# Optimization experiments

Hardware: AMD Instinct MI355X
Metric: run time of the kernel (lower is better)

The kernel has to match this reference:

```python
import jax, jax.numpy as jnp
import numpy as np

B, S, DM = 4, 2048, 512
H, D = 8, 64          # att_head, head_dim = att_dim // att_head
LEFT, RIGHT = 128, 128  # band_part(left_mask, right_mask)
LARGE = 1e30          # masked_softmax large number for fp32


def setup_inputs() -> dict:
    key = jax.random.key(0)
    ks = jax.random.split(key, 11)
    scale = 1.0 / np.sqrt(DM)
    x = jax.random.normal(ks[0], (B, S, DM), jnp.float32)
    Wq = jax.random.normal(ks[1], (DM, DM), jnp.float32) * scale
    bq = jnp.zeros((DM,), jnp.float32)
    Wk = jax.random.normal(ks[2], (DM, DM), jnp.float32) * scale
    bk = jnp.zeros((DM,), jnp.float32)
    Wv = jax.random.normal(ks[3], (DM, DM), jnp.float32) * scale
    bv = jnp.zeros((DM,), jnp.float32)
    Wo = jax.random.normal(ks[4], (DM, DM), jnp.float32) * scale
    bo = jnp.zeros((DM,), jnp.float32)
    x_len = jax.random.randint(ks[5], (B,), 0, 2048)
    return {"x": x, "Wq": Wq, "bq": bq, "Wk": Wk, "bk": bk,
            "Wv": Wv, "bv": bv, "Wo": Wo, "bo": bo, "x_len": x_len}


def reference(x, Wq, bq, Wk, bk, Wv, bv, Wo, bo, x_len):
    b, s, _ = x.shape
    # QKV projections, split into heads: [B,S,H,D]
    q = (x @ Wq + bq).reshape(b, s, H, D)
    k = (x @ Wk + bk).reshape(b, s, H, D)
    v = (x @ Wv + bv).reshape(b, s, H, D)
    # content energy: [B,H,Q,K], scaled by sqrt(head_dim)
    energy = jnp.einsum('bind,bjnd->bnij', q, k) / jnp.sqrt(jnp.float32(D))
    # banded mask (tf.linalg.band_part semantics): keep -LEFT <= j-i <= RIGHT
    i = jnp.arange(s)[:, None]
    j = jnp.arange(s)[None, :]
    band = ((j - i) <= RIGHT) & ((i - j) <= LEFT)            # [S,S]
    # key-length mask (tf.sequence_mask, expanded to [B,1,1,S])
    seq = jnp.arange(s)[None, :] < x_len[:, None]            # [B,S]
    mask = (band[None, None, :, :] & seq[:, None, None, :]).astype(energy.dtype)
    # masked softmax: energy - (1 - mask) * LARGE, softmax over keys
    att = jax.nn.softmax(energy - (1.0 - mask) * LARGE, axis=-1)
    # context: [B,Q,H,D] -> [B,S,H*D]
    ctx = jnp.einsum('bnij,bjnd->bind', att, v).reshape(b, s, H * D)
    # output projection (use_proj=True)
    return ctx @ Wo + bo
```

## Files before the change

kernel.cpp:

```cpp
#include <hip/hip_runtime.h>

#define S_LEN 2048
#define BATCH 4
#define DMODEL 512
#define NHEAD 8
#define HDIM 64
#define ROWS (BATCH * S_LEN)

using short8 = __attribute__((ext_vector_type(8))) short;
using f32x4  = __attribute__((ext_vector_type(4))) float;

__device__ __forceinline__ unsigned short f2bf(float f) {
  unsigned int u = __builtin_bit_cast(unsigned int, f);
  u += 0x7fffu + ((u >> 16) & 1u);
  return (unsigned short)(u >> 16);
}
__device__ __forceinline__ float bf2f(unsigned short h) {
  unsigned int u = ((unsigned int)h) << 16;
  return __builtin_bit_cast(float, u);
}
__device__ __forceinline__ void glds16(const void* g, void* l) {
  __builtin_amdgcn_global_load_lds((const __attribute__((address_space(1))) unsigned*)g,
                                   (__attribute__((address_space(3))) unsigned*)l, 16, 0, 0);
}

__global__ __launch_bounds__(256) void prep_kernel(const float* __restrict__ x,
                                                   const float* __restrict__ Wq,
                                                   const float* __restrict__ Wk,
                                                   const float* __restrict__ Wv,
                                                   const float* __restrict__ Wo,
                                                   unsigned short* __restrict__ xb,
                                                   unsigned short* __restrict__ WqkT,
                                                   unsigned short* __restrict__ WvT,
                                                   unsigned short* __restrict__ WoT) {
  __shared__ float t[32][33];
  const int blk = blockIdx.x, tid = threadIdx.x;
  if (blk < 2048) {
    const int base = (blk * 256 + tid) * 8;
    float4 f0 = *(const float4*)(x + base);
    float4 f1 = *(const float4*)(x + base + 4);
    uint4 o;
    o.x = (unsigned)f2bf(f0.x) | ((unsigned)f2bf(f0.y) << 16);
    o.y = (unsigned)f2bf(f0.z) | ((unsigned)f2bf(f0.w) << 16);
    o.z = (unsigned)f2bf(f1.x) | ((unsigned)f2bf(f1.y) << 16);
    o.w = (unsigned)f2bf(f1.z) | ((unsigned)f2bf(f1.w) << 16);
    *(uint4*)(xb + base) = o;
    return;
  }
  const int tb = blk - 2048;
  const int which = tb >> 8;
  const int tile = tb & 255;
  const float* W = which == 0 ? Wq : which == 1 ? Wk : which == 2 ? Wv : Wo;
  unsigned short* WT = which == 0 ? WqkT : which == 1 ? (WqkT + 512 * 512)
                      : which == 2 ? WvT : WoT;
  const int tx = tid & 31, ty = tid >> 5;
  const int x0 = (tile & 15) * 32, y0 = (tile >> 4) * 32;
#pragma unroll
  for (int r = 0; r < 4; r++)
    t[ty + 8 * r][tx] = W[(size_t)(y0 + ty + 8 * r) * DMODEL + x0 + tx];
  __syncthreads();
#pragma unroll
  for (int r = 0; r < 4; r++)
    WT[(size_t)(x0 + ty + 8 * r) * DMODEL + y0 + tx] = f2bf(t[tx][ty + 8 * r]);
}

__global__ __launch_bounds__(256, 2) void gemm_qkv_kernel(const unsigned short* __restrict__ xb,
                                                          const unsigned short* __restrict__ WqkT,
                                                          const unsigned short* __restrict__ WvT,
                                                          const float* __restrict__ bq,
                                                          const float* __restrict__ bk,
                                                          const float* __restrict__ bv,
                                                          const int* __restrict__ x_len,
                                                          unsigned short* __restrict__ Qb,
                                                          unsigned short* __restrict__ Kb,
                                                          unsigned short* __restrict__ Vt) {
  constexpr int K = DMODEL;
  __shared__ __align__(16) char smem[16384];
  char* As = smem;
  char* Bs = smem + 8192;
  const int bid = blockIdx.x;
  const bool vmode = bid < 256;
  const unsigned short *A, *Bt;
  int m0, n0;
  if (vmode) {
    m0 = (bid & 3) * 128;
    n0 = (bid >> 2) * 128;
    A = WvT; Bt = xb;
  } else {
    const int q = bid - 256;
    m0 = (q >> 3) * 128;
    n0 = (q & 7) * 128;
    A = xb; Bt = WqkT;
    const int xl = x_len[m0 >> 11];
    const int s0 = m0 & 2047;
    if (n0 >= DMODEL) { if (s0 >= xl) return; }
    else if (s0 >= xl + 128) return;
  }
  const int tid = threadIdx.x;
  const int wave = tid >> 6, lane = tid & 63;
  const int wr = wave >> 1, wc = wave & 1;
  const int lm = lane & 15, lq = lane >> 4;
  const int lr = lane >> 2;
  const int lc = (lane & 3) ^ ((lane >> 3) & 3);
  const unsigned short* gA0 = A + (size_t)(m0 + wave * 16 + lr) * K + lc * 8;
  const unsigned short* gA1 = A + (size_t)(m0 + (wave + 4) * 16 + lr) * K + lc * 8;
  const unsigned short* gB0 = Bt + (size_t)(n0 + wave * 16 + lr) * K + lc * 8;
  const unsigned short* gB1 = Bt + (size_t)(n0 + (wave + 4) * 16 + lr) * K + lc * 8;
  char* lA0 = As + wave * 1024 + lane * 16;
  char* lA1 = As + (wave + 4) * 1024 + lane * 16;
  char* lB0 = Bs + wave * 1024 + lane * 16;
  char* lB1 = Bs + (wave + 4) * 1024 + lane * 16;
  const int sw = (lm >> 1) & 3;
  int aoff[4], boff[4];
#pragma unroll
  for (int mi = 0; mi < 4; mi++)
    aoff[mi] = (wr * 64 + mi * 16 + lm) * 64 + (lq ^ sw) * 16;
#pragma unroll
  for (int ni = 0; ni < 4; ni++)
    boff[ni] = (wc * 64 + ni * 16 + lm) * 64 + (lq ^ sw) * 16;

  f32x4 acc[4][4] = {};
  for (int k0 = 0; k0 < K; k0 += 32) {
    __syncthreads();
    glds16(gA0 + k0, lA0);
    glds16(gA1 + k0, lA1);
    glds16(gB0 + k0, lB0);
    glds16(gB1 + k0, lB1);
    __syncthreads();
    short8 af[4], bfr[4];
#pragma unroll
    for (int mi = 0; mi < 4; mi++) af[mi] = *(const short8*)(As + aoff[mi]);
#pragma unroll
    for (int ni = 0; ni < 4; ni++) bfr[ni] = *(const short8*)(Bs + boff[ni]);
#pragma unroll
    for (int mi = 0; mi < 4; mi++)
#pragma unroll
      for (int ni = 0; ni < 4; ni++)
        acc[mi][ni] = __builtin_amdgcn_mfma_f32_16x16x32_bf16(af[mi], bfr[ni], acc[mi][ni], 0, 0, 0);
  }
#pragma unroll
  for (int mi = 0; mi < 4; mi++) {
    const int row0 = m0 + wr * 64 + mi * 16 + lq * 4;
#pragma unroll
    for (int ni = 0; ni < 4; ni++) {
      const int col = n0 + wc * 64 + ni * 16 + lm;
#pragma unroll
      for (int r = 0; r < 4; r++) {
        const int row = row0 + r;
        const float v = acc[mi][ni][r];
        if (vmode) {
          Vt[(size_t)row * ROWS + col] = f2bf(v + bv[row]);
        } else if (col < DMODEL) {
          Qb[(size_t)row * DMODEL + col] = f2bf(v + bq[col]);
        } else {
          Kb[(size_t)row * DMODEL + (col - DMODEL)] = f2bf(v + bk[col - DMODEL]);
        }
      }
    }
  }
}

__global__ __launch_bounds__(256, 2) void gemm_out_kernel(const unsigned short* __restrict__ A,
                                                          const unsigned short* __restrict__ Bt,
                                                          const float* __restrict__ bias,
                                                          float* __restrict__ out) {
  constexpr int K = DMODEL;
  __shared__ __align__(16) char smem[16384];
  char* As = smem;
  char* Bs = smem + 8192;
  const int tid = threadIdx.x;
  const int wave = tid >> 6, lane = tid & 63;
  const int wr = wave >> 1, wc = wave & 1;
  const int lm = lane & 15, lq = lane >> 4;
  const int m0 = blockIdx.y * 128, n0 = blockIdx.x * 128;
  const int lr = lane >> 2;
  const int lc = (lane & 3) ^ ((lane >> 3) & 3);
  const unsigned short* gA0 = A + (size_t)(m0 + wave * 16 + lr) * K + lc * 8;
  const unsigned short* gA1 = A + (size_t)(m0 + (wave + 4) * 16 + lr) * K + lc * 8;
  const unsigned short* gB0 = Bt + (size_t)(n0 + wave * 16 + lr) * K + lc * 8;
  const unsigned short* gB1 = Bt + (size_t)(n0 + (wave + 4) * 16 + lr) * K + lc * 8;
  char* lA0 = As + wave * 1024 + lane * 16;
  char* lA1 = As + (wave + 4) * 1024 + lane * 16;
  char* lB0 = Bs + wave * 1024 + lane * 16;
  char* lB1 = Bs + (wave + 4) * 1024 + lane * 16;
  const int sw = (lm >> 1) & 3;
  int aoff[4], boff[4];
#pragma unroll
  for (int mi = 0; mi < 4; mi++)
    aoff[mi] = (wr * 64 + mi * 16 + lm) * 64 + (lq ^ sw) * 16;
#pragma unroll
  for (int ni = 0; ni < 4; ni++)
    boff[ni] = (wc * 64 + ni * 16 + lm) * 64 + (lq ^ sw) * 16;

  f32x4 acc[4][4] = {};
  for (int k0 = 0; k0 < K; k0 += 32) {
    __syncthreads();
    glds16(gA0 + k0, lA0);
    glds16(gA1 + k0, lA1);
    glds16(gB0 + k0, lB0);
    glds16(gB1 + k0, lB1);
    __syncthreads();
    short8 af[4], bfr[4];
#pragma unroll
    for (int mi = 0; mi < 4; mi++) af[mi] = *(const short8*)(As + aoff[mi]);
#pragma unroll
    for (int ni = 0; ni < 4; ni++) bfr[ni] = *(const short8*)(Bs + boff[ni]);
#pragma unroll
    for (int mi = 0; mi < 4; mi++)
#pragma unroll
      for (int ni = 0; ni < 4; ni++)
        acc[mi][ni] = __builtin_amdgcn_mfma_f32_16x16x32_bf16(af[mi], bfr[ni], acc[mi][ni], 0, 0, 0);
  }
#pragma unroll
  for (int mi = 0; mi < 4; mi++) {
    const int row0 = m0 + wr * 64 + mi * 16 + lq * 4;
#pragma unroll
    for (int ni = 0; ni < 4; ni++) {
      const int col = n0 + wc * 64 + ni * 16 + lm;
#pragma unroll
      for (int r = 0; r < 4; r++)
        out[(size_t)(row0 + r) * DMODEL + col] = acc[mi][ni][r] + bias[col];
    }
  }
}

__global__ __launch_bounds__(256) void vsum_kernel(const unsigned short* __restrict__ Vt,
                                                   float* __restrict__ vs) {
  const int wid = blockIdx.x * 4 + (threadIdx.x >> 6);
  const int lane = threadIdx.x & 63;
  const int b = wid >> 9, n = wid & 511;
  const unsigned short* row = Vt + (size_t)n * ROWS + b * S_LEN;
  float s = 0.f;
#pragma unroll
  for (int it = 0; it < 4; it++) {
    uint4 v = *(const uint4*)(row + it * 512 + lane * 8);
    unsigned int w[4] = {v.x, v.y, v.z, v.w};
#pragma unroll
    for (int e = 0; e < 4; e++) {
      s += bf2f((unsigned short)(w[e] & 0xffffu));
      s += bf2f((unsigned short)(w[e] >> 16));
    }
  }
#pragma unroll
  for (int off = 1; off < 64; off <<= 1) s += __shfl_xor(s, off, 64);
  if (lane == 0) vs[(size_t)b * DMODEL + n] = s;
}

__global__ __launch_bounds__(256) void attn_kernel(const unsigned short* __restrict__ Q,
                                                   const unsigned short* __restrict__ K,
                                                   const unsigned short* __restrict__ Vt,
                                                   const int* __restrict__ x_len,
                                                   const float* __restrict__ vsum,
                                                   unsigned short* __restrict__ ctx) {
  __shared__ unsigned short Ks[32][72];
  __shared__ unsigned short Vs[64][40];
  __shared__ unsigned short Ps[4][2][16][40];
  const int tid = threadIdx.x;
  const int wave = tid >> 6, lane = tid & 63;
  const int lm = lane & 15, lq = lane >> 4;
  const int b = blockIdx.z, h = blockIdx.y;
  const int i0 = blockIdx.x * 128;
  const int qbase = i0 + wave * 32;
  const int xlen = x_len[b];

  short8 aq[2][2];
#pragma unroll
  for (int g = 0; g < 2; g++) {
    const size_t qoff = (size_t)(b * S_LEN + qbase + g * 16 + lm) * DMODEL + h * HDIM + lq * 8;
    aq[g][0] = *(const short8*)(Q + qoff);
    aq[g][1] = *(const short8*)(Q + qoff + 32);
  }

  const int krow = tid >> 3, kchk = (tid & 7) * 8;
  const int vdim = tid >> 2, vchk = (tid & 3) * 8;

  f32x4 oacc[2][4] = {};
  float mrow[2][4], lrow[2][4];
#pragma unroll
  for (int g = 0; g < 2; g++)
#pragma unroll
    for (int r = 0; r < 4; r++) { mrow[g][r] = -1e30f; lrow[g][r] = 0.f; }

  for (int kt = 0; kt < 12; kt++) {
    const int jt0 = i0 - 128 + kt * 32;
    if (jt0 + 31 < 0 || jt0 >= xlen) continue;
    __syncthreads();
    {
      const int jr = jt0 + krow;
      const int jrc = min(max(jr, 0), S_LEN - 1);
      *(uint4*)&Ks[krow][kchk] =
          *(const uint4*)(K + (size_t)(b * S_LEN + jrc) * DMODEL + h * HDIM + kchk);
      const int jv = jt0 + vchk;
      const int jvc = min(max(jv, 0), S_LEN - 8);
      *(uint4*)&Vs[vdim][vchk] =
          *(const uint4*)(Vt + (size_t)(h * HDIM + vdim) * ROWS + b * S_LEN + jvc);
    }
    __syncthreads();
    if (jt0 + 159 < qbase || jt0 > qbase + 159) continue;

#pragma unroll
    for (int g = 0; g < 2; g++) {
      const int qg = qbase + g * 16;
      if (jt0 + 31 < qg - 128 || jt0 > qg + 143) continue;
      f32x4 sv[2];
#pragma unroll
      for (int sub = 0; sub < 2; sub++) {
        const short8 bk0 = *(const short8*)&Ks[sub * 16 + lm][lq * 8];
        const short8 bk1 = *(const short8*)&Ks[sub * 16 + lm][32 + lq * 8];
        f32x4 s = {};
        s = __builtin_amdgcn_mfma_f32_16x16x32_bf16(aq[g][0], bk0, s, 0, 0, 0);
        s = __builtin_amdgcn_mfma_f32_16x16x32_bf16(aq[g][1], bk1, s, 0, 0, 0);
        sv[sub] = s;
      }
#pragma unroll
      for (int sub = 0; sub < 2; sub++) {
        const int j = jt0 + sub * 16 + lm;
        const bool jv = (j >= 0) && (j < xlen);
#pragma unroll
        for (int r = 0; r < 4; r++) {
          const int i = qg + lq * 4 + r;
          const bool ok = jv && (j - i <= 128) && (i - j <= 128);
          sv[sub][r] = ok ? sv[sub][r] * 0.125f : -1e30f;
        }
      }
      float alpha[4], p0[4], p1[4];
#pragma unroll
      for (int r = 0; r < 4; r++) {
        float mx = fmaxf(sv[0][r], sv[1][r]);
#pragma unroll
        for (int off = 1; off < 16; off <<= 1) mx = fmaxf(mx, __shfl_xor(mx, off, 64));
        const float mn = fmaxf(mrow[g][r], mx);
        alpha[r] = __expf(mrow[g][r] - mn);
        mrow[g][r] = mn;
        p0[r] = (sv[0][r] > -1e29f) ? __expf(sv[0][r] - mn) : 0.f;
        p1[r] = (sv[1][r] > -1e29f) ? __expf(sv[1][r] - mn) : 0.f;
        float rs = p0[r] + p1[r];
#pragma unroll
        for (int off = 1; off < 16; off <<= 1) rs += __shfl_xor(rs, off, 64);
        lrow[g][r] = lrow[g][r] * alpha[r] + rs;
      }
#pragma unroll
      for (int r = 0; r < 4; r++) {
        Ps[wave][g][lq * 4 + r][lm] = f2bf(p0[r]);
        Ps[wave][g][lq * 4 + r][16 + lm] = f2bf(p1[r]);
      }
      const short8 pf = *(const short8*)&Ps[wave][g][lm][lq * 8];
#pragma unroll
      for (int dt = 0; dt < 4; dt++) {
#pragma unroll
        for (int r = 0; r < 4; r++) oacc[g][dt][r] *= alpha[r];
        const short8 bv = *(const short8*)&Vs[dt * 16 + lm][lq * 8];
        oacc[g][dt] = __builtin_amdgcn_mfma_f32_16x16x32_bf16(pf, bv, oacc[g][dt], 0, 0, 0);
      }
    }
  }
#pragma unroll
  for (int g = 0; g < 2; g++)
#pragma unroll
    for (int r = 0; r < 4; r++) {
      const int i = qbase + g * 16 + lq * 4 + r;
      const size_t obase = (size_t)(b * S_LEN + i) * DMODEL + h * HDIM;
      if (lrow[g][r] > 0.f) {
        const float inv = 1.f / lrow[g][r];
#pragma unroll
        for (int dt = 0; dt < 4; dt++)
          ctx[obase + dt * 16 + lm] = f2bf(oacc[g][dt][r] * inv);
      } else {
#pragma unroll
        for (int dt = 0; dt < 4; dt++)
          ctx[obase + dt * 16 + lm] =
              f2bf(vsum[(size_t)b * DMODEL + h * HDIM + dt * 16 + lm] * (1.f / 2048.f));
      }
    }
}

extern "C" void kernel_launch(void* const* d_in, const int* in_sizes, int n_in,
                              void* d_out, int out_size, void* d_ws, size_t ws_size,
                              hipStream_t stream) {
  (void)in_sizes; (void)n_in; (void)out_size; (void)ws_size;
  const float* x  = (const float*)d_in[0];
  const float* Wq = (const float*)d_in[1];
  const float* bq = (const float*)d_in[2];
  const float* Wk = (const float*)d_in[3];
  const float* bk = (const float*)d_in[4];
  const float* Wv = (const float*)d_in[5];
  const float* bv = (const float*)d_in[6];
  const float* Wo = (const float*)d_in[7];
  const float* bo = (const float*)d_in[8];
  const int* x_len = (const int*)d_in[9];

  char* ws = (char*)d_ws;
  const size_t MB = 1024 * 1024;
  unsigned short* xb   = (unsigned short*)(ws + 0 * MB);
  unsigned short* Qb   = (unsigned short*)(ws + 8 * MB);
  unsigned short* Kb   = (unsigned short*)(ws + 16 * MB);
  unsigned short* Vt   = (unsigned short*)(ws + 24 * MB);
  unsigned short* Cx   = (unsigned short*)(ws + 32 * MB);
  unsigned short* WqkT = (unsigned short*)(ws + 40 * MB);
  unsigned short* WvT  = (unsigned short*)(ws + 41 * MB);
  unsigned short* WoT  = (unsigned short*)(ws + 41 * MB + 512 * 1024);
  float* vsum          = (float*)(ws + 42 * MB);

  prep_kernel<<<3072, 256, 0, stream>>>(x, Wq, Wk, Wv, Wo, xb, WqkT, WvT, WoT);
  gemm_qkv_kernel<<<768, 256, 0, stream>>>(xb, WqkT, WvT, bq, bk, bv, x_len, Qb, Kb, Vt);
  vsum_kernel<<<512, 256, 0, stream>>>(Vt, vsum);
  attn_kernel<<<dim3(16, 8, 4), 256, 0, stream>>>(Qb, Kb, Vt, x_len, vsum, Cx);
  gemm_out_kernel<<<dim3(4, 64), 256, 0, stream>>>(Cx, WoT, bo, (float*)d_out);
}
```

Measured before the change: 170.8 us.

## Drop online-softmax max tracking and shrink attention blocks to 64 queries

The banded attention kernel stops tracking a running row maximum. It exponentiates the scaled scores directly, with no rescaling of accumulators and no per-tile shuffle reductions, and does a single sum reduction at the end. Each block now covers 64 queries with one 16-row group per wave, and the grid doubles so the band loop runs over 10 key tiles instead of 12. This removes the per-tile max/sum shuffles and the accumulator rescaling, and raises parallelism. The trade-offs are more redundant K/V tile loads across blocks and a risk of exp overflow if scores are large.

```diff
diff --git a/kernel.cpp b/kernel.cpp
--- a/kernel.cpp
+++ b/kernel.cpp
@@ -254,34 +254,26 @@
                                                    unsigned short* __restrict__ ctx) {
   __shared__ unsigned short Ks[32][72];
   __shared__ unsigned short Vs[64][40];
-  __shared__ unsigned short Ps[4][2][16][40];
+  __shared__ unsigned short Ps[4][16][40];
   const int tid = threadIdx.x;
   const int wave = tid >> 6, lane = tid & 63;
   const int lm = lane & 15, lq = lane >> 4;
   const int b = blockIdx.z, h = blockIdx.y;
-  const int i0 = blockIdx.x * 128;
-  const int qbase = i0 + wave * 32;
+  const int i0 = blockIdx.x * 64;
+  const int q0 = i0 + wave * 16;
   const int xlen = x_len[b];
 
-  short8 aq[2][2];
-#pragma unroll
-  for (int g = 0; g < 2; g++) {
-    const size_t qoff = (size_t)(b * S_LEN + qbase + g * 16 + lm) * DMODEL + h * HDIM + lq * 8;
-    aq[g][0] = *(const short8*)(Q + qoff);
-    aq[g][1] = *(const short8*)(Q + qoff + 32);
-  }
+  const size_t qoff = (size_t)(b * S_LEN + q0 + lm) * DMODEL + h * HDIM + lq * 8;
+  const short8 aq0 = *(const short8*)(Q + qoff);
+  const short8 aq1 = *(const short8*)(Q + qoff + 32);
 
   const int krow = tid >> 3, kchk = (tid & 7) * 8;
   const int vdim = tid >> 2, vchk = (tid & 3) * 8;
 
-  f32x4 oacc[2][4] = {};
-  float mrow[2][4], lrow[2][4];
-#pragma unroll
-  for (int g = 0; g < 2; g++)
-#pragma unroll
-    for (int r = 0; r < 4; r++) { mrow[g][r] = -1e30f; lrow[g][r] = 0.f; }
-
-  for (int kt = 0; kt < 12; kt++) {
+  f32x4 oacc[4] = {};
+  float lrow[4] = {0.f, 0.f, 0.f, 0.f};
+
+  for (int kt = 0; kt < 10; kt++) {
     const int jt0 = i0 - 128 + kt * 32;
     if (jt0 + 31 < 0 || jt0 >= xlen) continue;
     __syncthreads();
@@ -296,82 +288,65 @@
           *(const uint4*)(Vt + (size_t)(h * HDIM + vdim) * ROWS + b * S_LEN + jvc);
     }
     __syncthreads();
-    if (jt0 + 159 < qbase || jt0 > qbase + 159) continue;
-
-#pragma unroll
-    for (int g = 0; g < 2; g++) {
-      const int qg = qbase + g * 16;
-      if (jt0 + 31 < qg - 128 || jt0 > qg + 143) continue;
-      f32x4 sv[2];
-#pragma unroll
-      for (int sub = 0; sub < 2; sub++) {
-        const short8 bk0 = *(const short8*)&Ks[sub * 16 + lm][lq * 8];
-        const short8 bk1 = *(const short8*)&Ks[sub * 16 + lm][32 + lq * 8];
-        f32x4 s = {};
-        s = __builtin_amdgcn_mfma_f32_16x16x32_bf16(aq[g][0], bk0, s, 0, 0, 0);
-        s = __builtin_amdgcn_mfma_f32_16x16x32_bf16(aq[g][1], bk1, s, 0, 0, 0);
-        sv[sub] = s;
+    if (jt0 + 31 < q0 - 128 || jt0 > q0 + 143) continue;
+
+    f32x4 sv[2];
+#pragma unroll
+    for (int sub = 0; sub < 2; sub++) {
+      const short8 bk0 = *(const short8*)&Ks[sub * 16 + lm][lq * 8];
+      const short8 bk1 = *(const short8*)&Ks[sub * 16 + lm][32 + lq * 8];
+      f32x4 s = {};
+      s = __builtin_amdgcn_mfma_f32_16x16x32_bf16(aq0, bk0, s, 0, 0, 0);
+      s = __builtin_amdgcn_mfma_f32_16x16x32_bf16(aq1, bk1, s, 0, 0, 0);
+      sv[sub] = s;
+    }
+    float p[2][4];
+#pragma unroll
+    for (int sub = 0; sub < 2; sub++) {
+      const int j = jt0 + sub * 16 + lm;
+      const bool jv = (j >= 0) && (j < xlen);
+#pragma unroll
+      for (int r = 0; r < 4; r++) {
+        const int i = q0 + lq * 4 + r;
+        const bool ok = jv && (j - i <= 128) && (i - j <= 128);
+        const float pv = ok ? __expf(sv[sub][r] * 0.125f) : 0.f;
+        p[sub][r] = pv;
+        lrow[r] += pv;
       }
-#pragma unroll
-      for (int sub = 0; sub < 2; sub++) {
-        const int j = jt0 + sub * 16 + lm;
-        const bool jv = (j >= 0) && (j < xlen);
-#pragma unroll
-        for (int r = 0; r < 4; r++) {
-          const int i = qg + lq * 4 + r;
-          const bool ok = jv && (j - i <= 128) && (i - j <= 128);
-          sv[sub][r] = ok ? sv[sub][r] * 0.125f : -1e30f;
-        }
-      }
-      float alpha[4], p0[4], p1[4];
-#pragma unroll
-      for (int r = 0; r < 4; r++) {
-        float mx = fmaxf(sv[0][r], sv[1][r]);
-#pragma unroll
-        for (int off = 1; off < 16; off <<= 1) mx = fmaxf(mx, __shfl_xor(mx, off, 64));
-        const float mn = fmaxf(mrow[g][r], mx);
-        alpha[r] = __expf(mrow[g][r] - mn);
-        mrow[g][r] = mn;
-        p0[r] = (sv[0][r] > -1e29f) ? __expf(sv[0][r] - mn) : 0.f;
-        p1[r] = (sv[1][r] > -1e29f) ? __expf(sv[1][r] - mn) : 0.f;
-        float rs = p0[r] + p1[r];
-#pragma unroll
-        for (int off = 1; off < 16; off <<= 1) rs += __shfl_xor(rs, off, 64);
-        lrow[g][r] = lrow[g][r] * alpha[r] + rs;
-      }
-#pragma unroll
-      for (int r = 0; r < 4; r++) {
-        Ps[wave][g][lq * 4 + r][lm] = f2bf(p0[r]);
-        Ps[wave][g][lq * 4 + r][16 + lm] = f2bf(p1[r]);
-      }
-      const short8 pf = *(const short8*)&Ps[wave][g][lm][lq * 8];
-#pragma unroll
-      for (int dt = 0; dt < 4; dt++) {
-#pragma unroll
-        for (int r = 0; r < 4; r++) oacc[g][dt][r] *= alpha[r];
-        const short8 bv = *(const short8*)&Vs[dt * 16 + lm][lq * 8];
-        oacc[g][dt] = __builtin_amdgcn_mfma_f32_16x16x32_bf16(pf, bv, oacc[g][dt], 0, 0, 0);
-      }
-    }
-  }
-#pragma unroll
-  for (int g = 0; g < 2; g++)
+    }
 #pragma unroll
     for (int r = 0; r < 4; r++) {
-      const int i = qbase + g * 16 + lq * 4 + r;
-      const size_t obase = (size_t)(b * S_LEN + i) * DMODEL + h * HDIM;
-      if (lrow[g][r] > 0.f) {
-        const float inv = 1.f / lrow[g][r];
-#pragma unroll
-        for (int dt = 0; dt < 4; dt++)
-          ctx[obase + dt * 16 + lm] = f2bf(oacc[g][dt][r] * inv);
-      } else {
-#pragma unroll
-        for (int dt = 0; dt < 4; dt++)
-          ctx[obase + dt * 16 + lm] =
-              f2bf(vsum[(size_t)b * DMODEL + h * HDIM + dt * 16 + lm] * (1.f / 2048.f));
-      }
-    }
+      Ps[wave][lq * 4 + r][lm] = f2bf(p[0][r]);
+      Ps[wave][lq * 4 + r][16 + lm] = f2bf(p[1][r]);
+    }
+    const short8 pf = *(const short8*)&Ps[wave][lm][lq * 8];
+#pragma unroll
+    for (int dt = 0; dt < 4; dt++) {
+      const short8 bv = *(const short8*)&Vs[dt * 16 + lm][lq * 8];
+      oacc[dt] = __builtin_amdgcn_mfma_f32_16x16x32_bf16(pf, bv, oacc[dt], 0, 0, 0);
+    }
+  }
+#pragma unroll
+  for (int r = 0; r < 4; r++)
+#pragma unroll
+    for (int off = 1; off < 16; off <<= 1) lrow[r] += __shfl_xor(lrow[r], off, 64);
+
+#pragma unroll
+  for (int r = 0; r < 4; r++) {
+    const int i = q0 + lq * 4 + r;
+    const size_t obase = (size_t)(b * S_LEN + i) * DMODEL + h * HDIM;
+    if (lrow[r] > 0.f) {
+      const float inv = 1.f / lrow[r];
+#pragma unroll
+      for (int dt = 0; dt < 4; dt++)
+        ctx[obase + dt * 16 + lm] = f2bf(oacc[dt][r] * inv);
+    } else {
+#pragma unroll
+      for (int dt = 0; dt < 4; dt++)
+        ctx[obase + dt * 16 + lm] =
+            f2bf(vsum[(size_t)b * DMODEL + h * HDIM + dt * 16 + lm] * (1.f / 2048.f));
+    }
+  }
 }
 
 extern "C" void kernel_launch(void* const* d_in, const int* in_sizes, int n_in,
@@ -404,6 +379,6 @@
   prep_kernel<<<3072, 256, 0, stream>>>(x, Wq, Wk, Wv, Wo, xb, WqkT, WvT, WoT);
   gemm_qkv_kernel<<<768, 256, 0, stream>>>(xb, WqkT, WvT, bq, bk, bv, x_len, Qb, Kb, Vt);
   vsum_kernel<<<512, 256, 0, stream>>>(Vt, vsum);
-  attn_kernel<<<dim3(16, 8, 4), 256, 0, stream>>>(Qb, Kb, Vt, x_len, vsum, Cx);
+  attn_kernel<<<dim3(32, 8, 4), 256, 0, stream>>>(Qb, Kb, Vt, x_len, vsum, Cx);
   gemm_out_kernel<<<dim3(4, 64), 256, 0, stream>>>(Cx, WoT, bo, (float*)d_out);
 }
```

Measured after the change: 149.3 us. 12.6% less time.
